# Performance work log

Measured on AMD Instinct MI355X. Metric: run time of the kernel, lower is better.

Reference implementation:

```python
import jax, jax.numpy as jnp
import numpy as np

MODEL_DIM = 1024
N_Q_HEADS = 16
N_GROUPS = 4
KV_PER_Q = N_Q_HEADS // N_GROUPS        # 4
HEAD_DIM = MODEL_DIM // N_Q_HEADS       # 64
KV_HEAD_DIM = MODEL_DIM // KV_PER_Q     # 256 (per-group K/V total width = N_GROUPS*HEAD_DIM)
ROPE_THETA = 50000.0


def rope_cos_sin(seq_len, dim, dtype):
    # standard RoPE tables: [S, dim]
    inv_freq = 1.0 / (ROPE_THETA ** (jnp.arange(0, dim, 2, dtype=jnp.float32) / dim))
    freqs = jnp.arange(seq_len, dtype=jnp.float32)[:, None] * inv_freq[None, :]  # [S, dim/2]
    emb = jnp.concatenate([freqs, freqs], axis=-1)                               # [S, dim]
    return jnp.cos(emb).astype(dtype), jnp.sin(emb).astype(dtype)


def rotate_half(x):
    h = x.shape[-1] // 2
    return jnp.concatenate([-x[..., h:], x[..., :h]], axis=-1)


def setup_inputs() -> dict:
    key = jax.random.key(0)
    k0, k1, k2, k3, k4 = jax.random.split(key, 5)
    B, S = 2, 2048
    qkv_out = MODEL_DIM + 2 * KV_HEAD_DIM  # 1536
    s_in = 1.0 / np.sqrt(MODEL_DIM)
    return {
        "x": jax.random.normal(k0, (B, S, MODEL_DIM), jnp.float32),
        "W_qkv": jax.random.normal(k1, (MODEL_DIM, qkv_out), jnp.float32) * s_in,
        "b_qkv": jnp.zeros((qkv_out,), jnp.float32),
        "W_out": jax.random.normal(k2, (MODEL_DIM, MODEL_DIM), jnp.float32) * s_in,
        "b_out": jnp.zeros((MODEL_DIM,), jnp.float32),
    }


def reference(x, W_qkv, b_qkv, W_out, b_out):
    B, S, _ = x.shape
    fused = x @ W_qkv + b_qkv  # [B,S,MODEL_DIM + 2*KV_HEAD_DIM]
    q, k, v = jnp.split(fused, [MODEL_DIM, MODEL_DIM + KV_HEAD_DIM], axis=-1)

    # [B,S,(NH HD)] -> [B,NH,S,HD]
    q = q.reshape(B, S, N_Q_HEADS, HEAD_DIM).transpose(0, 2, 1, 3)
    k = k.reshape(B, S, N_GROUPS, HEAD_DIM).transpose(0, 2, 1, 3)
    v = v.reshape(B, S, N_GROUPS, HEAD_DIM).transpose(0, 2, 1, 3)

    cos, sin = rope_cos_sin(S, HEAD_DIM, x.dtype)  # [S,HD]
    cos = cos[None, None]                          # [1,1,S,HD]
    sin = sin[None, None]
    q = q * cos + rotate_half(q) * sin
    k = k * cos + rotate_half(k) * sin

    # GQA without materializing duplicated heads: group queries [B,G,R,S,HD]
    qg = q.reshape(B, N_GROUPS, KV_PER_Q, S, HEAD_DIM)
    scale = 1.0 / np.sqrt(HEAD_DIM)
    scores = jnp.einsum('bgrsh,bgth->bgrst', qg, k) * scale  # [B,G,R,S,S]
    causal = jnp.tril(jnp.ones((S, S), bool))
    scores = jnp.where(causal, scores, jnp.finfo(scores.dtype).min)
    probs = jax.nn.softmax(scores, axis=-1)
    out = jnp.einsum('bgrst,bgth->bgrsh', probs, v)          # [B,G,R,S,HD]

    # [B,G,R,S,HD] -> [B,S,MODEL_DIM]  (head index = g*R + r, matching duplicate_heads)
    out = out.reshape(B, N_Q_HEADS, S, HEAD_DIM).transpose(0, 2, 1, 3).reshape(B, S, MODEL_DIM)
    return out @ W_out + b_out
```

## Files before the change

### kernel.cpp

```cpp
#include <hip/hip_runtime.h>
#include <hip/hip_bf16.h>

typedef __attribute__((ext_vector_type(8))) short short8;
typedef __attribute__((ext_vector_type(4))) float f32x4;

__device__ __forceinline__ short tobf(float f) {
  __hip_bfloat16 h = __float2bfloat16(f);
  return *reinterpret_cast<short*>(&h);
}
__device__ __forceinline__ float frombf(short s) {
  unsigned u = ((unsigned)(unsigned short)s) << 16;
  return __uint_as_float(u);
}

__device__ __forceinline__ int swz(int row) { return (row ^ (row >> 3)) & 7; }

#define GLDS16(gp, lp) __builtin_amdgcn_global_load_lds( \
    (__attribute__((address_space(1))) void*)(gp),       \
    (__attribute__((address_space(3))) void*)(lp), 16, 0, 0)

__device__ __forceinline__ float exp2raw(float x) {
  float r;
  asm("v_exp_f32 %0, %1" : "=v"(r) : "v"(x));
  return r;
}
__device__ __forceinline__ unsigned cvtpk(float lo, float hi) {
  unsigned r;
  asm("v_cvt_pk_bf16_f32 %0, %1, %2" : "=v"(r) : "v"(lo), "v"(hi));
  return r;
}

#define QSCALE 0.18033688011112042f

__global__ __launch_bounds__(256) void prep_k(
    const float* __restrict__ x, short* __restrict__ xb,
    const float* __restrict__ Wqkv, short* __restrict__ WqkvT,
    const float* __restrict__ Wout, short* __restrict__ WoutT,
    float* __restrict__ cost, float* __restrict__ sint) {
  __shared__ float t[64][65];
  const int bx = blockIdx.x, tid = threadIdx.x;
  if (bx < 1024) {
    int base = bx * 4096 + tid * 4;
#pragma unroll
    for (int rep = 0; rep < 4; ++rep) {
      int i = base + rep * 1024;
      float4 v = *(const float4*)(x + i);
      *(short4*)(xb + i) = make_short4(tobf(v.x), tobf(v.y), tobf(v.z), tobf(v.w));
    }
  } else if (bx < 1664) {
    const float* in;
    short* out;
    int C, bb;
    if (bx < 1408) { in = Wqkv; out = WqkvT; C = 1536; bb = bx - 1024; }
    else           { in = Wout; out = WoutT; C = 1024; bb = bx - 1408; }
    const int R = 1024;
    int nc = C >> 6;
    int br = bb / nc, bc = bb % nc;
    int lr = tid >> 6, lc = tid & 63;
#pragma unroll
    for (int j = 0; j < 16; ++j) {
      int r = j * 4 + lr;
      t[r][lc] = in[(size_t)(br * 64 + r) * C + bc * 64 + lc];
    }
    __syncthreads();
#pragma unroll
    for (int j = 0; j < 16; ++j) {
      int r = j * 4 + lr;
      out[(size_t)(bc * 64 + r) * R + br * 64 + lc] = tobf(t[lc][r]);
    }
  } else {
    int t2 = (bx - 1664) * 256 + tid;
    int s = t2 >> 5, f = t2 & 31;
    float inv = __expf(-(float)f * (logf(50000.0f) / 32.0f));
    float a = (float)s * inv;
    cost[t2] = cosf(a);
    sint[t2] = sinf(a);
  }
}

template <int MODE>
__global__ __launch_bounds__(256) void gemm_k(
    const short* __restrict__ A, const short* __restrict__ Bt,
    const float* __restrict__ bias, void* __restrict__ Cout,
    short* __restrict__ vT,
    int M, int N, int K,
    const float* __restrict__ cost, const float* __restrict__ sint) {
  __shared__ short As[128 * 64];
  __shared__ short Bs[64 * 64];
  const int ntile = N >> 6;
  const int bm = blockIdx.x / ntile, bn = blockIdx.x % ntile;
  const int tid = threadIdx.x, w = tid >> 6, l = tid & 63;
  const int c = l & 15, g = l >> 4;
  const int m0 = bm * 128, n0 = bn * 64;

  f32x4 acc[2][4] = {};

  for (int k0 = 0; k0 < K; k0 += 64) {
#pragma unroll
    for (int j = 0; j < 4; ++j) {
      int rb = j * 32 + w * 8;
      int row = rb + (l >> 3);
      int colel = ((l & 7) ^ swz(row)) * 8;
      GLDS16(A + (size_t)(m0 + row) * K + k0 + colel, &As[rb * 64]);
      if (j < 2) GLDS16(Bt + (size_t)(n0 + row) * K + k0 + colel, &Bs[rb * 64]);
    }
    __syncthreads();
#pragma unroll
    for (int kk = 0; kk < 2; ++kk) {
      short8 af[2], bf[4];
#pragma unroll
      for (int mi = 0; mi < 2; ++mi) {
        int row = w * 32 + mi * 16 + c;
        af[mi] = *(const short8*)&As[row * 64 + ((kk * 4 + g) ^ swz(row)) * 8];
      }
#pragma unroll
      for (int ni = 0; ni < 4; ++ni) {
        int row = ni * 16 + c;
        bf[ni] = *(const short8*)&Bs[row * 64 + ((kk * 4 + g) ^ swz(row)) * 8];
      }
#pragma unroll
      for (int mi = 0; mi < 2; ++mi)
#pragma unroll
        for (int ni = 0; ni < 4; ++ni)
          acc[mi][ni] = __builtin_amdgcn_mfma_f32_16x16x32_bf16(af[mi], bf[ni], acc[mi][ni], 0, 0, 0);
    }
    __syncthreads();
  }

  if (MODE == 0 && n0 >= 1280) {
    const int hg = (n0 - 1280) >> 6;
#pragma unroll
    for (int mi = 0; mi < 2; ++mi) {
      int m0r = m0 + w * 32 + mi * 16 + g * 4;
      int b = m0r >> 11, s = m0r & 2047;
#pragma unroll
      for (int ni = 0; ni < 4; ++ni) {
        int d = ni * 16 + c;
        float bs = bias[n0 + d];
        short4 o;
        o.x = tobf(acc[mi][ni][0] + bs);
        o.y = tobf(acc[mi][ni][1] + bs);
        o.z = tobf(acc[mi][ni][2] + bs);
        o.w = tobf(acc[mi][ni][3] + bs);
        *(short4*)&vT[(size_t)((b * 4 + hg) * 64 + d) * 2048 + s] = o;
      }
    }
    return;
  }

#pragma unroll
  for (int mi = 0; mi < 2; ++mi)
#pragma unroll
    for (int r = 0; r < 4; ++r) {
      int m = m0 + w * 32 + mi * 16 + g * 4 + r;
      int s = m & 2047;
#pragma unroll
      for (int ni = 0; ni < 4; ++ni) {
        int n = n0 + ni * 16 + c;
        float v = acc[mi][ni][r] + bias[n];
        if (MODE == 0) {
          int d = n & 63, f = d & 31;
          float cs = cost[s * 32 + f], sn = sint[s * 32 + f];
          float partner = acc[mi][ni ^ 2][r] + bias[n ^ 32];
          v = (d < 32) ? (v * cs - partner * sn) : (v * cs + partner * sn);
          if (n < 1024) v *= QSCALE;
          ((short*)Cout)[(size_t)m * N + n] = tobf(v);
        } else {
          ((float*)Cout)[(size_t)m * N + n] = v;
        }
      }
    }
}

__global__ __launch_bounds__(512) void attn_k(const short* __restrict__ qkv,
                                              const short* __restrict__ vT,
                                              short* __restrict__ pacc,
                                              float* __restrict__ plrun) {
  __shared__ short Ks3[3][64 * 64];
  __shared__ short Vt3[3][64 * 64];
  __shared__ short Ps[8][16 * 64];

  const int bx = blockIdx.x;
  const int bh = bx & 31;
  const int rest = bx >> 5;
  const int p = rest & 3;
  const int half = rest >> 2;
  const int qtB = 7 - p, qtA = p;
  const int sB = 32 - 4 * p;
  const int start = half * 18;
  const int end = start + 18;
  const int b = bh >> 4, h = bh & 15, hg = h >> 2;
  const int tid = threadIdx.x, w = tid >> 6, l = tid & 63;
  const int c = l & 15, g = l >> 4;
  const size_t rowbase = (size_t)(b * 2048) * 1536;

  const int srow = w * 8 + (l >> 3);
  const int scol = ((l & 7) ^ swz(srow)) * 8;
  const size_t koff = (size_t)srow * 1536 + scol;
  const size_t voff = (size_t)srow * 2048 + scol;
  const int ldsoff = (w * 8) * 64;
  const short* kbase = qkv + rowbase + 1024 + hg * 64;
  const short* vbase_p = vT + (size_t)((b * 4 + hg) * 64) * 2048;

#define KTOF(i) (((i) < sB) ? (i) : ((i) - sB))

  {
    int t0 = KTOF(start), t1 = KTOF(start + 1);
    GLDS16(kbase + (size_t)t0 * 98304 + koff, &Ks3[0][ldsoff]);
    GLDS16(vbase_p + t0 * 64 + voff, &Vt3[0][ldsoff]);
    GLDS16(kbase + (size_t)t1 * 98304 + koff, &Ks3[1][ldsoff]);
    GLDS16(vbase_p + t1 * 64 + voff, &Vt3[1][ldsoff]);
  }
  asm volatile("s_waitcnt vmcnt(2)" ::: "memory");
  __builtin_amdgcn_s_barrier();
  __builtin_amdgcn_sched_barrier(0);

  f32x4 acco[2][4] = {};
  float lrun[2] = {0.f, 0.f};
  short* Pw = &Ps[w][0];
  short8 aq[2][2];
  int cur = 0, s2 = 2;

#pragma unroll
  for (int set = 0; set < 2; ++set)
#pragma unroll
    for (int kk = 0; kk < 2; ++kk)
      aq[set][kk] = *(const short8*)(qkv + rowbase +
          (size_t)(qtB * 256 + w * 32 + set * 16 + c) * 1536 + h * 64 + kk * 32 + g * 8);

#define BODY(qtc)                                                               \
  {                                                                             \
    const int kt = KTOF(i);                                                     \
    const bool pf2 = (i + 2 < end);                                             \
    if (pf2) {         \
      int ktp = KTOF(i + 2);                                                    \
      GLDS16(kbase + (size_t)ktp * 98304 + koff, &Ks3[s2][ldsoff]);             \
      GLDS16(vbase_p + ktp * 64 + voff, &Vt3[s2][ldsoff]);                      \
    }                                                                           \
    short8 bk[2][4];                                                            \
    _Pragma("unroll") for (int kk = 0; kk < 2; ++kk)                            \
      _Pragma("unroll") for (int nb = 0; nb < 4; ++nb) {                        \
        int row = nb * 16 + c;                                                  \
        bk[kk][nb] = *(const short8*)&Ks3[cur][row * 64 + ((kk * 4 + g) ^ swz(row)) * 8]; \
      }                                                                         \
    f32x4 sfr[2][4] = {};                                                       \
    __builtin_amdgcn_s_setprio(1);                                              \
    _Pragma("unroll") for (int set = 0; set < 2; ++set)                         \
      _Pragma("unroll") for (int kk = 0; kk < 2; ++kk)                          \
        _Pragma("unroll") for (int nb = 0; nb < 4; ++nb)                        \
          sfr[set][nb] = __builtin_amdgcn_mfma_f32_16x16x32_bf16(               \
              bk[kk][nb], aq[set][kk], sfr[set][nb], 0, 0, 0);                  \
    __builtin_amdgcn_s_setprio(0);                                              \
    short8 bv[2][4];                                                            \
    _Pragma("unroll") for (int kk = 0; kk < 2; ++kk)                            \
      _Pragma("unroll") for (int nb = 0; nb < 4; ++nb) {                        \
        int row = nb * 16 + c;                                                  \
        bv[kk][nb] = *(const short8*)&Vt3[cur][row * 64 + ((kk * 4 + g) ^ swz(row)) * 8]; \
      }                                                                         \
    if (kt >= 4 * (qtc)) {            \
      _Pragma("unroll") for (int set = 0; set < 2; ++set) {                     \
        int qg = (qtc)*256 + w * 32 + set * 16 + c;                             \
        _Pragma("unroll") for (int nb = 0; nb < 4; ++nb)                        \
          _Pragma("unroll") for (int r = 0; r < 4; ++r)                         \
            if (kt * 64 + nb * 16 + g * 4 + r > qg) sfr[set][nb][r] = -1e30f;   \
      }                                                                         \
    }                                                                           \
    _Pragma("unroll") for (int set = 0; set < 2; ++set) {                       \
      float rsn[4];                                                             \
      _Pragma("unroll") for (int nb = 0; nb < 4; ++nb) {                        \
        float p0 = exp2raw(sfr[set][nb][0]);                                    \
        float p1 = exp2raw(sfr[set][nb][1]);                                    \
        float p2 = exp2raw(sfr[set][nb][2]);                                    \
        float p3 = exp2raw(sfr[set][nb][3]);                                    \
        sfr[set][nb][0] = p0; sfr[set][nb][1] = p1;                             \
        sfr[set][nb][2] = p2; sfr[set][nb][3] = p3;                             \
        rsn[nb] = (p0 + p1) + (p2 + p3);                                        \
      }                                                                         \
      lrun[set] += (rsn[0] + rsn[1]) + (rsn[2] + rsn[3]);                       \
      _Pragma("unroll") for (int nb = 0; nb < 4; ++nb) {                        \
        unsigned d0 = cvtpk(sfr[set][nb][0], sfr[set][nb][1]);                  \
        unsigned d1 = cvtpk(sfr[set][nb][2], sfr[set][nb][3]);                  \
        int pslot = (nb * 2 + (g >> 1)) ^ swz(c);                               \
        int2 pq2 = make_int2((int)d0, (int)d1);                                 \
        *(int2*)&Pw[c * 64 + pslot * 8 + (g & 1) * 4] = pq2;                    \
      }                                                                         \
      __builtin_amdgcn_s_setprio(1);                                            \
      _Pragma("unroll") for (int kk = 0; kk < 2; ++kk) {                        \
        short8 ap = *(const short8*)&Pw[c * 64 + (((kk * 4 + g) ^ swz(c)) * 8)];\
        _Pragma("unroll") for (int nb = 0; nb < 4; ++nb)                        \
          acco[set][nb] = __builtin_amdgcn_mfma_f32_16x16x32_bf16(              \
              ap, bv[kk][nb], acco[set][nb], 0, 0, 0);                          \
      }                                                                         \
      __builtin_amdgcn_s_setprio(0);                                            \
    }                                                                           \
    if (pf2) asm volatile("s_waitcnt vmcnt(2)" ::: "memory");                   \
    else     asm volatile("s_waitcnt vmcnt(0)" ::: "memory");                   \
    __builtin_amdgcn_s_barrier();                                               \
    __builtin_amdgcn_sched_barrier(0);                                          \
    cur = (cur == 2) ? 0 : cur + 1;                                             \
    s2 = (s2 == 2) ? 0 : s2 + 1;                                                \
  }

#define STORE_PARTIAL(slot)                                                     \
  {                                                                             \
    int sidx = ((bh * 4 + p) * 2 + half) * 2 + (slot);                          \
    size_t pb = (size_t)sidx * 16384;                                           \
    _Pragma("unroll") for (int set = 0; set < 2; ++set) {                       \
      _Pragma("unroll") for (int nb = 0; nb < 4; ++nb)                          \
        _Pragma("unroll") for (int r = 0; r < 4; ++r) {                         \
          int row = w * 32 + set * 16 + g * 4 + r;                              \
          pacc[pb + row * 64 + nb * 16 + c] = tobf(acco[set][nb][r]);           \
          acco[set][nb][r] = 0.f;                                               \
        }                                                                       \
      float lr_ = lrun[set];                                                    \
      lr_ += __shfl_xor(lr_, 16, 64);                                           \
      lr_ += __shfl_xor(lr_, 32, 64);          \
      if (g == 0) plrun[sidx * 256 + w * 32 + set * 16 + c] = lr_;              \
      lrun[set] = 0.f;                                                          \
    }                                                                           \
  }

  int i = start;
  const int endB = (end < sB) ? end : sB;
  for (; i < endB; ++i) BODY(qtB);
  STORE_PARTIAL(0);

#pragma unroll
  for (int set = 0; set < 2; ++set)
#pragma unroll
    for (int kk = 0; kk < 2; ++kk)
      aq[set][kk] = *(const short8*)(qkv + rowbase +
          (size_t)(qtA * 256 + w * 32 + set * 16 + c) * 1536 + h * 64 + kk * 32 + g * 8);

  for (; i < end; ++i) BODY(qtA);
  STORE_PARTIAL(1);

#undef BODY
#undef STORE_PARTIAL
#undef KTOF
}

__global__ __launch_bounds__(256) void combine_k(const short* __restrict__ pacc,
                                                 const float* __restrict__ plrun,
                                                 short* __restrict__ attnb) {
  int e = blockIdx.x * 256 + threadIdx.x;
  int d8 = e & 7;
  int t = e >> 3;
  int row = t & 255;
  int t2 = t >> 8;
  int qt = t2 & 7;
  int bh = t2 >> 3;
  int p = (qt < 7 - qt) ? qt : 7 - qt;
  int slot = (qt >= 4) ? 0 : 1;
  float acc[8] = {};
  float lsum = 0.f;
#pragma unroll
  for (int half = 0; half < 2; ++half) {
    int sidx = ((bh * 4 + p) * 2 + half) * 2 + slot;
    short8 a = *(const short8*)(pacc + (size_t)sidx * 16384 + row * 64 + d8 * 8);
#pragma unroll
    for (int k = 0; k < 8; ++k) acc[k] += frombf(a[k]);
    lsum += plrun[sidx * 256 + row];
  }
  float li = 1.0f / lsum;
  int b = bh >> 4, h = bh & 15;
  int m = b * 2048 + qt * 256 + row;
  int n = h * 64 + d8 * 8;
  short8 o;
#pragma unroll
  for (int k = 0; k < 8; ++k) o[k] = tobf(acc[k] * li);
  *(short8*)(attnb + (size_t)m * 1024 + n) = o;
}

extern "C" void kernel_launch(void* const* d_in, const int* in_sizes, int n_in,
                              void* d_out, int out_size, void* d_ws, size_t ws_size,
                              hipStream_t stream) {
  const float* x    = (const float*)d_in[0];
  const float* Wqkv = (const float*)d_in[1];
  const float* bqkv = (const float*)d_in[2];
  const float* Wout = (const float*)d_in[3];
  const float* bout = (const float*)d_in[4];

  char* ws = (char*)d_ws;
  short* pacc  = (short*)(ws + 0);
  short* xb    = (short*)(ws + 0);
  short* WqkvT = (short*)(ws + 8388608);
  float* cost  = (float*)(ws + 11534336);
  float* sint  = (float*)(ws + 11796480);
  short* WoutT = (short*)(ws + 33554432);
  short* qkvb  = (short*)(ws + 35651584);
  short* attnb = (short*)(ws + 35651584);
  short* vTb   = (short*)(ws + 48234496);
  float* plrun = (float*)(ws + 50331648);

  prep_k<<<1920, 256, 0, stream>>>(x, xb, Wqkv, WqkvT, Wout, WoutT, cost, sint);
  gemm_k<0><<<768, 256, 0, stream>>>(xb, WqkvT, bqkv, (void*)qkvb, vTb, 4096, 1536, 1024, cost, sint);
  attn_k<<<256, 512, 0, stream>>>(qkvb, vTb, pacc, plrun);
  combine_k<<<2048, 256, 0, stream>>>(pacc, plrun, attnb);
  gemm_k<1><<<512, 256, 0, stream>>>(attnb, WoutT, bout, d_out, nullptr, 4096, 1024, 1024, cost, sint);
}
```

Measured before the change: 91.86 us.

## Process two K/V tiles per barrier with six-deep LDS ring buffer

The attention kernel's K/V LDS ring grows from three to six tile buffers. Each loop iteration now computes two key tiles between barriers and prefetches the next pair four tiles ahead. The aim is to halve the number of block barriers and waitcnt stalls and to hide more global-load latency. In exchange LDS use per block roughly doubles, which can lower how many blocks fit on a CU. The loop also relies on the tile ranges always having even length.

```diff
diff --git a/kernel.cpp b/kernel.cpp
--- a/kernel.cpp
+++ b/kernel.cpp
@@ -176,8 +176,8 @@
                                               const short* __restrict__ vT,
                                               short* __restrict__ pacc,
                                               float* __restrict__ plrun) {
-  __shared__ short Ks3[3][64 * 64];
-  __shared__ short Vt3[3][64 * 64];
+  __shared__ short Ks6[6][64 * 64];
+  __shared__ short Vt6[6][64 * 64];
   __shared__ short Ps[8][16 * 64];
 
   const int bx = blockIdx.x;
@@ -204,14 +204,15 @@
 
 #define KTOF(i) (((i) < sB) ? (i) : ((i) - sB))
 
-  {
-    int t0 = KTOF(start), t1 = KTOF(start + 1);
-    GLDS16(kbase + (size_t)t0 * 98304 + koff, &Ks3[0][ldsoff]);
-    GLDS16(vbase_p + t0 * 64 + voff, &Vt3[0][ldsoff]);
-    GLDS16(kbase + (size_t)t1 * 98304 + koff, &Ks3[1][ldsoff]);
-    GLDS16(vbase_p + t1 * 64 + voff, &Vt3[1][ldsoff]);
-  }
-  asm volatile("s_waitcnt vmcnt(2)" ::: "memory");
+#pragma unroll
+  for (int t = 0; t < 4; ++t) {
+    int idx = start + t;
+    int kt0 = KTOF(idx);
+    int bf_ = idx % 6;
+    GLDS16(kbase + (size_t)kt0 * 98304 + koff, &Ks6[bf_][ldsoff]);
+    GLDS16(vbase_p + kt0 * 64 + voff, &Vt6[bf_][ldsoff]);
+  }
+  asm volatile("s_waitcnt vmcnt(4)" ::: "memory");
   __builtin_amdgcn_s_barrier();
   __builtin_amdgcn_sched_barrier(0);
 
@@ -219,7 +220,6 @@
   float lrun[2] = {0.f, 0.f};
   short* Pw = &Ps[w][0];
   short8 aq[2][2];
-  int cur = 0, s2 = 2;
 
 #pragma unroll
   for (int set = 0; set < 2; ++set)
@@ -228,20 +228,15 @@
       aq[set][kk] = *(const short8*)(qkv + rowbase +
           (size_t)(qtB * 256 + w * 32 + set * 16 + c) * 1536 + h * 64 + kk * 32 + g * 8);
 
-#define BODY(qtc)                                                               \
+#define CORE(qtc, TI)                                                           \
   {                                                                             \
-    const int kt = KTOF(i);                                                     \
-    const bool pf2 = (i + 2 < end);                                             \
-    if (pf2) {         \
-      int ktp = KTOF(i + 2);                                                    \
-      GLDS16(kbase + (size_t)ktp * 98304 + koff, &Ks3[s2][ldsoff]);             \
-      GLDS16(vbase_p + ktp * 64 + voff, &Vt3[s2][ldsoff]);                      \
-    }                                                                           \
+    const int kt_ = KTOF(TI);                                                   \
+    const int bf_ = (TI) % 6;                                                   \
     short8 bk[2][4];                                                            \
     _Pragma("unroll") for (int kk = 0; kk < 2; ++kk)                            \
       _Pragma("unroll") for (int nb = 0; nb < 4; ++nb) {                        \
         int row = nb * 16 + c;                                                  \
-        bk[kk][nb] = *(const short8*)&Ks3[cur][row * 64 + ((kk * 4 + g) ^ swz(row)) * 8]; \
+        bk[kk][nb] = *(const short8*)&Ks6[bf_][row * 64 + ((kk * 4 + g) ^ swz(row)) * 8]; \
       }                                                                         \
     f32x4 sfr[2][4] = {};                                                       \
     __builtin_amdgcn_s_setprio(1);                                              \
@@ -255,14 +250,14 @@
     _Pragma("unroll") for (int kk = 0; kk < 2; ++kk)                            \
       _Pragma("unroll") for (int nb = 0; nb < 4; ++nb) {                        \
         int row = nb * 16 + c;                                                  \
-        bv[kk][nb] = *(const short8*)&Vt3[cur][row * 64 + ((kk * 4 + g) ^ swz(row)) * 8]; \
-      }                                                                         \
-    if (kt >= 4 * (qtc)) {            \
+        bv[kk][nb] = *(const short8*)&Vt6[bf_][row * 64 + ((kk * 4 + g) ^ swz(row)) * 8]; \
+      }                                                                         \
+    if (kt_ >= 4 * (qtc)) {           \
       _Pragma("unroll") for (int set = 0; set < 2; ++set) {                     \
         int qg = (qtc)*256 + w * 32 + set * 16 + c;                             \
         _Pragma("unroll") for (int nb = 0; nb < 4; ++nb)                        \
           _Pragma("unroll") for (int r = 0; r < 4; ++r)                         \
-            if (kt * 64 + nb * 16 + g * 4 + r > qg) sfr[set][nb][r] = -1e30f;   \
+            if (kt_ * 64 + nb * 16 + g * 4 + r > qg) sfr[set][nb][r] = -1e30f;  \
       }                                                                         \
     }                                                                           \
     _Pragma("unroll") for (int set = 0; set < 2; ++set) {                       \
@@ -293,12 +288,25 @@
       }                                                                         \
       __builtin_amdgcn_s_setprio(0);                                            \
     }                                                                           \
-    if (pf2) asm volatile("s_waitcnt vmcnt(2)" ::: "memory");                   \
+  }
+
+#define SUPER(qtc)                                                              \
+  {                                                                             \
+    const bool pf_ = (i + 4 < end);                                             \
+    if (pf_) {                                                                  \
+      int ta = KTOF(i + 4), tb = KTOF(i + 5);                                   \
+      int ba = (i + 4) % 6, bb2 = (i + 5) % 6;                                  \
+      GLDS16(kbase + (size_t)ta * 98304 + koff, &Ks6[ba][ldsoff]);              \
+      GLDS16(vbase_p + ta * 64 + voff, &Vt6[ba][ldsoff]);                       \
+      GLDS16(kbase + (size_t)tb * 98304 + koff, &Ks6[bb2][ldsoff]);             \
+      GLDS16(vbase_p + tb * 64 + voff, &Vt6[bb2][ldsoff]);                      \
+    }                                                                           \
+    CORE(qtc, i);                                                               \
+    CORE(qtc, i + 1);                                                           \
+    if (pf_) asm volatile("s_waitcnt vmcnt(4)" ::: "memory");                   \
     else     asm volatile("s_waitcnt vmcnt(0)" ::: "memory");                   \
     __builtin_amdgcn_s_barrier();                                               \
     __builtin_amdgcn_sched_barrier(0);                                          \
-    cur = (cur == 2) ? 0 : cur + 1;                                             \
-    s2 = (s2 == 2) ? 0 : s2 + 1;                                                \
   }
 
 #define STORE_PARTIAL(slot)                                                     \
@@ -322,7 +330,7 @@
 
   int i = start;
   const int endB = (end < sB) ? end : sB;
-  for (; i < endB; ++i) BODY(qtB);
+  for (; i < endB; i += 2) SUPER(qtB);
   STORE_PARTIAL(0);
 
 #pragma unroll
@@ -332,10 +340,11 @@
       aq[set][kk] = *(const short8*)(qkv + rowbase +
           (size_t)(qtA * 256 + w * 32 + set * 16 + c) * 1536 + h * 64 + kk * 32 + g * 8);
 
-  for (; i < end; ++i) BODY(qtA);
+  for (; i < end; i += 2) SUPER(qtA);
   STORE_PARTIAL(1);
 
-#undef BODY
+#undef CORE
+#undef SUPER
 #undef STORE_PARTIAL
 #undef KTOF
 }
```

Result: faster. 89.09 us, median of 2 (-3.0%).
